# Optimization experiments

Measured on AMD Instinct MI355X. Metric: run time of the kernel, lower is better.

## Reference

```python
import jax, jax.numpy as jnp
import numpy as np

DIM = 1024
NUM_HEADS = 16
HEAD_DIM = DIM // NUM_HEADS
SCALE = HEAD_DIM ** -0.5


def setup_inputs() -> dict:
    key = jax.random.key(0)
    ks = jax.random.split(key, 6)
    B, N = 2, 2048
    s = DIM ** -0.5
    return {
        "x": jax.random.normal(ks[0], (B, N, DIM), dtype=jnp.float32),
        "Wq": jax.random.normal(ks[1], (DIM, DIM), dtype=jnp.float32) * s,
        "Wk": jax.random.normal(ks[2], (DIM, DIM), dtype=jnp.float32) * s,
        "Wv": jax.random.normal(ks[3], (DIM, DIM), dtype=jnp.float32) * s,
        "Wp": jax.random.normal(ks[4], (DIM, DIM), dtype=jnp.float32) * s,
        "bp": jax.random.normal(ks[5], (DIM,), dtype=jnp.float32) * 0.01,
    }


def reference(x, Wq, Wk, Wv, Wp, bp):
    B, N, C = x.shape
    H, D = NUM_HEADS, HEAD_DIM
    # projections (torch Linear: x @ W.T); reshape to (B, H, N, D)
    q = (x @ Wq.T).reshape(B, N, H, D).transpose(0, 2, 1, 3)
    k = (x @ Wk.T).reshape(B, N, H, D).transpose(0, 2, 1, 3)
    v = (x @ Wv.T).reshape(B, N, H, D).transpose(0, 2, 1, 3)
    attn = jnp.einsum("bhnd,bhmd->bhnm", q, k) * SCALE
    attn = jax.nn.softmax(attn, axis=-1)  # dropout p=0 -> identity
    out = jnp.einsum("bhnm,bhmd->bhnd", attn, v)
    out = out.transpose(0, 2, 1, 3).reshape(B, N, C)
    return out @ Wp.T + bp
```

## Files before the change

kernel.cpp:

```cpp
#include <hip/hip_runtime.h>
#include <cstdint>

#define DIMC   1024
#define NHEADS 16
#define HD     64
#define BATCH  2
#define SEQ    2048
#define MROWS  (BATCH*SEQ)
#define QSCALE2 0.18033688f

typedef __bf16 bf16x8 __attribute__((ext_vector_type(8)));
typedef float  f32x4  __attribute__((ext_vector_type(4)));

#define AST 88
#define TST 136

__device__ __forceinline__ unsigned short f2bf(float f) {
    union { float f; unsigned int u; } v; v.f = f;
    unsigned int u = v.u;
    u += 0x7fffu + ((u >> 16) & 1u);
    return (unsigned short)(u >> 16);
}

__device__ __forceinline__ unsigned int pk2bf(float a, float b) {
    union { float f; unsigned int u; } ua, ub;
    ua.f = a; ub.f = b;
    return __builtin_amdgcn_perm(ub.u + 0x8000u, ua.u + 0x8000u, 0x07060302u);
}

__device__ __forceinline__ void gload_lds16(const void* g, void* l) {
    __builtin_amdgcn_global_load_lds(
        (const __attribute__((address_space(1))) unsigned int*)g,
        (__attribute__((address_space(3))) unsigned int*)l, 16, 0, 0);
}

__global__ __launch_bounds__(256) void cast_all(
    const float* __restrict__ x,
    const float* __restrict__ Wq, const float* __restrict__ Wk,
    const float* __restrict__ Wv, const float* __restrict__ Wp,
    unsigned short* __restrict__ xb, unsigned short* __restrict__ Wb)
{
    const size_t M1 = (size_t)DIMC * DIMC;
    int y = blockIdx.y;
    const float* src;
    unsigned short* dst;
    if (y < 4)      { src = x  + (size_t)y * M1; dst = xb + (size_t)y * M1; }
    else if (y == 4){ src = Wq; dst = Wb; }
    else if (y == 5){ src = Wk; dst = Wb + M1; }
    else if (y == 6){ src = Wv; dst = Wb + 2 * M1; }
    else            { src = Wp; dst = Wb + 3 * M1; }
    size_t idx = ((size_t)blockIdx.x * 256 + threadIdx.x) * 4;
    float4 v = *(const float4*)(src + idx);
    ushort4 p; p.x = f2bf(v.x); p.y = f2bf(v.y); p.z = f2bf(v.z); p.w = f2bf(v.w);
    *(ushort4*)(dst + idx) = p;
}

__device__ __forceinline__ void gemm_issue(
    const unsigned short* __restrict__ A, const unsigned short* __restrict__ B,
    unsigned short* As, unsigned short* Bs, int m0, int n0, int kt)
{
    const int t = threadIdx.x;
    const int w = t >> 6, lane = t & 63;
    const int srow = lane >> 3, scol = lane & 7;
#pragma unroll
    for (int i = 0; i < 4; ++i) {
        int r  = i * 32 + w * 8 + srow;
        int cg = scol ^ (r & 7);
        gload_lds16(A + (size_t)(m0 + r) * DIMC + kt + cg * 8, As + r * 64 + scol * 8);
    }
#pragma unroll
    for (int i = 0; i < 2; ++i) {
        int r  = i * 32 + w * 8 + srow;
        int cg = scol ^ (r & 7);
        gload_lds16(B + (size_t)(n0 + r) * DIMC + kt + cg * 8, Bs + r * 64 + scol * 8);
    }
}

__device__ __forceinline__ void gemm_compute(
    const unsigned short* As, const unsigned short* Bs, f32x4 acc[4][2])
{
    const int t = threadIdx.x;
    const int w = t >> 6, lane = t & 63, quad = lane >> 4, lr = lane & 15;
    const int wr = w >> 1, wc = w & 1;
#pragma unroll
    for (int kk = 0; kk < 2; ++kk) {
        bf16x8 af[4], bfr[2];
#pragma unroll
        for (int mt = 0; mt < 4; ++mt) {
            int row = wr * 64 + mt * 16 + lr;
            int cb  = kk * 4 + quad;
            af[mt] = *(const bf16x8*)&As[row * 64 + (cb ^ (row & 7)) * 8];
        }
#pragma unroll
        for (int nt = 0; nt < 2; ++nt) {
            int row = wc * 32 + nt * 16 + lr;
            int cb  = kk * 4 + quad;
            bfr[nt] = *(const bf16x8*)&Bs[row * 64 + (cb ^ (row & 7)) * 8];
        }
#pragma unroll
        for (int mt = 0; mt < 4; ++mt)
#pragma unroll
            for (int nt = 0; nt < 2; ++nt)
                acc[mt][nt] = __builtin_amdgcn_mfma_f32_16x16x32_bf16(af[mt], bfr[nt], acc[mt][nt], 0, 0, 0);
    }
}

__device__ __forceinline__ void gemm_k_loop_db(
    const unsigned short* __restrict__ A, const unsigned short* __restrict__ B,
    unsigned short* smem, int m0, int n0, f32x4 acc[4][2])
{
    unsigned short* As0 = smem;
    unsigned short* Bs0 = smem + 8192;
    unsigned short* As1 = smem + 12288;
    unsigned short* Bs1 = smem + 20480;

    gemm_issue(A, B, As0, Bs0, m0, n0, 0);
    for (int kt = 0; kt < DIMC; kt += 128) {
        __syncthreads();
        gemm_issue(A, B, As1, Bs1, m0, n0, kt + 64);
        gemm_compute(As0, Bs0, acc);
        __syncthreads();
        if (kt + 128 < DIMC) gemm_issue(A, B, As0, Bs0, m0, n0, kt + 128);
        gemm_compute(As1, Bs1, acc);
    }
}

__device__ __forceinline__ void vt_epilogue(
    unsigned short* Ts, f32x4 acc[4][2], int m0, int n0,
    unsigned short* __restrict__ vT)
{
    const int t = threadIdx.x;
    const int w = t >> 6, lane = t & 63, quad = lane >> 4, lr = lane & 15;
    const int wr = w >> 1, wc = w & 1;

    __syncthreads();
#pragma unroll
    for (int mt = 0; mt < 4; ++mt)
#pragma unroll
        for (int nt = 0; nt < 2; ++nt) {
            int lcol  = wc * 32 + nt * 16 + lr;
            int lrow0 = wr * 64 + mt * 16 + quad * 4;
            ushort4 p;
            p.x = f2bf(acc[mt][nt][0]); p.y = f2bf(acc[mt][nt][1]);
            p.z = f2bf(acc[mt][nt][2]); p.w = f2bf(acc[mt][nt][3]);
            *(ushort4*)&Ts[lcol * TST + lrow0] = p;
        }
    __syncthreads();

    int lc = t >> 2, part = t & 3;
    int cg = n0 + lc, hh = cg >> 6, dd = cg & 63;
    int bb = m0 >> 11, nn0 = m0 & (SEQ - 1);
    size_t dst = ((size_t)((bb * NHEADS + hh) * HD + dd)) * SEQ + nn0 + part * 32;
    const unsigned short* srcp = &Ts[lc * TST + part * 32];
#pragma unroll
    for (int i = 0; i < 4; ++i)
        *(uint4*)&vT[dst + i * 8] = *(const uint4*)&srcp[i * 8];
}

__global__ __launch_bounds__(256, 3) void gemm_qkv_fast(
    const unsigned short* __restrict__ xb, const unsigned short* __restrict__ Wb,
    unsigned short* __restrict__ qo, unsigned short* __restrict__ ko,
    unsigned short* __restrict__ vT)
{
    __shared__ unsigned short smem[24576];

    const int t  = threadIdx.x;
    const int lin = blockIdx.y * 16 + blockIdx.x;
    const int T   = (lin & 7) * 64 + (lin >> 3);
    const int n0 = (T & 15) * 64, m0 = (T >> 4) * 128, z = blockIdx.z;
    const unsigned short* B = Wb + (size_t)z * DIMC * DIMC;
    const int w = t >> 6, lane = t & 63, quad = lane >> 4, lr = lane & 15;
    const int wr = w >> 1, wc = w & 1;

    f32x4 acc[4][2];
#pragma unroll
    for (int mt = 0; mt < 4; ++mt)
#pragma unroll
        for (int nt = 0; nt < 2; ++nt)
#pragma unroll
            for (int r = 0; r < 4; ++r) acc[mt][nt][r] = 0.f;

    gemm_k_loop_db(xb, B, smem, m0, n0, acc);

    if (z == 2) {
        vt_epilogue(smem, acc, m0, n0, vT);
    } else {
        unsigned short* Out = (z == 0) ? qo : ko;
        const float sc = (z == 0) ? QSCALE2 : 1.0f;
#pragma unroll
        for (int mt = 0; mt < 4; ++mt)
#pragma unroll
            for (int nt = 0; nt < 2; ++nt)
#pragma unroll
                for (int r = 0; r < 4; ++r) {
                    int row = m0 + wr * 64 + mt * 16 + quad * 4 + r;
                    int col = n0 + wc * 32 + nt * 16 + lr;
                    Out[(size_t)row * DIMC + col] = f2bf(acc[mt][nt][r] * sc);
                }
    }
}

__global__ __launch_bounds__(256, 3) void gemm_out_fast(
    const unsigned short* __restrict__ O, const unsigned short* __restrict__ Wpb,
    const float* __restrict__ bias, float* __restrict__ out)
{
    __shared__ unsigned short smem[24576];

    const int t  = threadIdx.x;
    const int lin = blockIdx.y * 16 + blockIdx.x;
    const int T   = (lin & 7) * 64 + (lin >> 3);
    const int n0 = (T & 15) * 64, m0 = (T >> 4) * 128;
    const int w = t >> 6, lane = t & 63, quad = lane >> 4, lr = lane & 15;
    const int wr = w >> 1, wc = w & 1;

    f32x4 acc[4][2];
#pragma unroll
    for (int mt = 0; mt < 4; ++mt)
#pragma unroll
        for (int nt = 0; nt < 2; ++nt)
#pragma unroll
            for (int r = 0; r < 4; ++r) acc[mt][nt][r] = 0.f;

    gemm_k_loop_db(O, Wpb, smem, m0, n0, acc);

#pragma unroll
    for (int mt = 0; mt < 4; ++mt)
#pragma unroll
        for (int nt = 0; nt < 2; ++nt)
#pragma unroll
            for (int r = 0; r < 4; ++r) {
                int row = m0 + wr * 64 + mt * 16 + quad * 4 + r;
                int col = n0 + wc * 32 + nt * 16 + lr;
                out[(size_t)row * DIMC + col] = acc[mt][nt][r] + bias[col];
            }
}

__global__ __launch_bounds__(256, 2) void attn_kernel(
    const unsigned short* __restrict__ qg, const unsigned short* __restrict__ kg,
    const unsigned short* __restrict__ vT, unsigned short* __restrict__ og)
{
    __shared__ unsigned short Ka[64 * 64];
    __shared__ unsigned short Kb[64 * 64];
    __shared__ unsigned short Va[64 * 64];
    __shared__ unsigned short Vb[64 * 64];
    __shared__ unsigned short PsA[128 * 64];
    __shared__ unsigned short PsB[128 * 64];

    const int t  = threadIdx.x;
    const int w = t >> 6, l = t & 63, quad = l >> 4, lr = l & 15;
    const int srow = t >> 3, scol = t & 7;
    const int pkey = (lr & 7) << 1;

    const int bid  = blockIdx.x;
    const int slot = bid >> 3;
    const int bh   = (bid & 7) * 4 + (slot >> 4);
    const int qt   = slot & 15;
    const int b    = bh >> 4, h = bh & 15;

    const unsigned short* khead = kg + ((size_t)(b * SEQ)) * DIMC + h * HD;
    const unsigned short* vhead = vT + (size_t)((b * NHEADS + h) * HD) * SEQ;

    bf16x8 qf[2][2];
#pragma unroll
    for (int mt = 0; mt < 2; ++mt) {
        const size_t qoff = ((size_t)(b * SEQ + qt * 128 + w * 32 + mt * 16 + lr)) * DIMC + h * HD;
        qf[mt][0] = *(const bf16x8*)(qg + qoff + 0  + quad * 8);
        qf[mt][1] = *(const bf16x8*)(qg + qoff + 32 + quad * 8);
    }

    bf16x8 ones;
#pragma unroll
    for (int j = 0; j < 8; ++j) ones[j] = (__bf16)1.0f;
    const f32x4 fzero = { 0.f, 0.f, 0.f, 0.f };

    f32x4 o_acc[2][4], lacc[2];
#pragma unroll
    for (int mt = 0; mt < 2; ++mt) {
        lacc[mt] = fzero;
#pragma unroll
        for (int ct = 0; ct < 4; ++ct) o_acc[mt][ct] = fzero;
    }

    auto issue = [&](int kt, unsigned short* Kd, unsigned short* Vd) {
#pragma unroll
        for (int i = 0; i < 2; ++i) {
            int r  = i * 32 + srow;
            int cg = scol ^ (r & 7);
            gload_lds16(khead + (size_t)(kt * 64 + r) * DIMC + cg * 8, Kd + r * 64 + scol * 8);
            gload_lds16(vhead + (size_t)r * SEQ + kt * 64 + cg * 8,   Vd + r * 64 + scol * 8);
        }
    };

    auto s_phase = [&](const unsigned short* Kc, f32x4 (&s)[2][4]) {
        __builtin_amdgcn_s_setprio(1);
#pragma unroll
        for (int nt = 0; nt < 4; ++nt) {
            int row = nt * 16 + lr;
            bf16x8 kf = *(const bf16x8*)&Kc[row * 64 + ((quad ^ (row & 7)) * 8)];
#pragma unroll
            for (int mt = 0; mt < 2; ++mt)
                s[mt][nt] = __builtin_amdgcn_mfma_f32_16x16x32_bf16(kf, qf[mt][0], fzero, 0, 0, 0);
        }
#pragma unroll
        for (int nt = 0; nt < 4; ++nt) {
            int row = nt * 16 + lr;
            bf16x8 kf = *(const bf16x8*)&Kc[row * 64 + (((4 + quad) ^ (row & 7)) * 8)];
#pragma unroll
            for (int mt = 0; mt < 2; ++mt)
                s[mt][nt] = __builtin_amdgcn_mfma_f32_16x16x32_bf16(kf, qf[mt][1], s[mt][nt], 0, 0, 0);
        }
        __builtin_amdgcn_s_setprio(0);
    };

    auto exp_store = [&](const f32x4 (&s)[2][4], unsigned short* PsW) {
#pragma unroll
        for (int mt = 0; mt < 2; ++mt)
#pragma unroll
            for (int nt = 0; nt < 4; ++nt) {
                uint2 pp;
                pp.x = pk2bf(__builtin_amdgcn_exp2f(s[mt][nt][0]),
                             __builtin_amdgcn_exp2f(s[mt][nt][1]));
                pp.y = pk2bf(__builtin_amdgcn_exp2f(s[mt][nt][2]),
                             __builtin_amdgcn_exp2f(s[mt][nt][3]));
                *(uint2*)&PsW[(w * 32 + mt * 16 + lr) * 64 + (((nt * 4 + quad) ^ pkey) * 4)] = pp;
            }
    };

    auto vload = [&](const unsigned short* Vc, bf16x8 (&vr)[8]) {
#pragma unroll
        for (int kk = 0; kk < 2; ++kk)
#pragma unroll
            for (int ct = 0; ct < 4; ++ct) {
                int row = ct * 16 + lr;
                vr[kk * 4 + ct] = *(const bf16x8*)&Vc[row * 64 + (((kk * 4 + quad) ^ (row & 7)) * 8)];
            }
    };

    auto pv = [&](const unsigned short* PsR, const bf16x8 (&vr)[8]) {
        __builtin_amdgcn_s_setprio(1);
#pragma unroll
        for (int kk = 0; kk < 2; ++kk)
#pragma unroll
            for (int mt = 0; mt < 2; ++mt) {
                bf16x8 pf = *(const bf16x8*)&PsR[(w * 32 + mt * 16 + lr) * 64 + (((kk * 8 + quad * 2) ^ pkey) * 4)];
                lacc[mt] = __builtin_amdgcn_mfma_f32_16x16x32_bf16(pf, ones, lacc[mt], 0, 0, 0);
#pragma unroll
                for (int ct = 0; ct < 4; ++ct)
                    o_acc[mt][ct] = __builtin_amdgcn_mfma_f32_16x16x32_bf16(pf, vr[kk * 4 + ct], o_acc[mt][ct], 0, 0, 0);
            }
        __builtin_amdgcn_s_setprio(0);
    };

    bf16x8 vrA[8], vrB[8];

    issue(0, Ka, Va);
    for (int kt = 0; kt < SEQ / 64; kt += 2) {
        __syncthreads();
        issue(kt + 1, Kb, Vb);
        {
            f32x4 s[2][4];
            s_phase(Ka, s);
            if (kt) pv(PsB, vrB);
            exp_store(s, PsA);
            vload(Va, vrA);
        }
        __syncthreads();
        if (kt + 2 < SEQ / 64) issue(kt + 2, Ka, Va);
        {
            f32x4 s[2][4];
            s_phase(Kb, s);
            pv(PsA, vrA);
            exp_store(s, PsB);
            vload(Vb, vrB);
        }
    }
    pv(PsB, vrB);

#pragma unroll
    for (int mt = 0; mt < 2; ++mt) {
        float inv[4];
#pragma unroll
        for (int r = 0; r < 4; ++r) inv[r] = 1.0f / lacc[mt][r];
#pragma unroll
        for (int ct = 0; ct < 4; ++ct)
#pragma unroll
            for (int r = 0; r < 4; ++r) {
                int qrow = qt * 128 + w * 32 + mt * 16 + quad * 4 + r;
                og[((size_t)(b * SEQ + qrow)) * DIMC + h * HD + ct * 16 + lr] =
                    f2bf(o_acc[mt][ct][r] * inv[r]);
            }
    }
}

__global__ __launch_bounds__(256) void gemm_qkv_f32(
    const float* __restrict__ x,
    const float* __restrict__ Wq, const float* __restrict__ Wk, const float* __restrict__ Wv,
    unsigned short* __restrict__ qo, unsigned short* __restrict__ ko, unsigned short* __restrict__ vT)
{
    __shared__ unsigned short smem[2 * 128 * AST];
    unsigned short* As = smem;
    unsigned short* Bs = smem + 128 * AST;

    const int t  = threadIdx.x;
    const int n0 = blockIdx.x * 128, m0 = blockIdx.y * 128, z = blockIdx.z;
    const float* W = (z == 0) ? Wq : (z == 1) ? Wk : Wv;
    const int w = t >> 6, l = t & 63, quad = l >> 4, lr = l & 15;
    const int wr = w >> 1, wc = w & 1;

    f32x4 acc[4][4];
#pragma unroll
    for (int mt = 0; mt < 4; ++mt)
#pragma unroll
        for (int nt = 0; nt < 4; ++nt)
#pragma unroll
            for (int r = 0; r < 4; ++r) acc[mt][nt][r] = 0.f;

    for (int kt = 0; kt < DIMC; kt += 64) {
        __syncthreads();
#pragma unroll
        for (int i = 0; i < 8; ++i) {
            int flat = t + i * 256;
            int row = flat >> 4, seg = flat & 15;
            float4 a = *(const float4*)(x + (size_t)(m0 + row) * DIMC + kt + seg * 4);
            ushort4 pa; pa.x = f2bf(a.x); pa.y = f2bf(a.y); pa.z = f2bf(a.z); pa.w = f2bf(a.w);
            *(ushort4*)&As[row * AST + seg * 4] = pa;
            float4 b = *(const float4*)(W + (size_t)(n0 + row) * DIMC + kt + seg * 4);
            ushort4 pb; pb.x = f2bf(b.x); pb.y = f2bf(b.y); pb.z = f2bf(b.z); pb.w = f2bf(b.w);
            *(ushort4*)&Bs[row * AST + seg * 4] = pb;
        }
        __syncthreads();
#pragma unroll
        for (int kk = 0; kk < 2; ++kk) {
            bf16x8 af[4], bfr[4];
#pragma unroll
            for (int mt = 0; mt < 4; ++mt)
                af[mt] = *(const bf16x8*)&As[(wr * 64 + mt * 16 + lr) * AST + kk * 32 + quad * 8];
#pragma unroll
            for (int nt = 0; nt < 4; ++nt)
                bfr[nt] = *(const bf16x8*)&Bs[(wc * 64 + nt * 16 + lr) * AST + kk * 32 + quad * 8];
#pragma unroll
            for (int mt = 0; mt < 4; ++mt)
#pragma unroll
                for (int nt = 0; nt < 4; ++nt)
                    acc[mt][nt] = __builtin_amdgcn_mfma_f32_16x16x32_bf16(af[mt], bfr[nt], acc[mt][nt], 0, 0, 0);
        }
    }

    if (z == 2) {
        __syncthreads();
#pragma unroll
        for (int mt = 0; mt < 4; ++mt)
#pragma unroll
            for (int nt = 0; nt < 4; ++nt) {
                int lcol  = wc * 64 + nt * 16 + lr;
                int lrow0 = wr * 64 + mt * 16 + quad * 4;
                ushort4 p;
                p.x = f2bf(acc[mt][nt][0]); p.y = f2bf(acc[mt][nt][1]);
                p.z = f2bf(acc[mt][nt][2]); p.w = f2bf(acc[mt][nt][3]);
                *(ushort4*)&smem[lcol * TST + lrow0] = p;
            }
        __syncthreads();
        int lc = t >> 1, half = t & 1;
        int cg = n0 + lc, hh = cg >> 6, dd = cg & 63;
        int bb = m0 >> 11, nn0 = m0 & (SEQ - 1);
        size_t dst = ((size_t)((bb * NHEADS + hh) * HD + dd)) * SEQ + nn0 + half * 64;
        const unsigned short* srcp = &smem[lc * TST + half * 64];
#pragma unroll
        for (int i = 0; i < 8; ++i)
            *(uint4*)&vT[dst + i * 8] = *(const uint4*)&srcp[i * 8];
    } else {
        unsigned short* Out = (z == 0) ? qo : ko;
        const float sc = (z == 0) ? QSCALE2 : 1.0f;
#pragma unroll
        for (int mt = 0; mt < 4; ++mt)
#pragma unroll
            for (int nt = 0; nt < 4; ++nt)
#pragma unroll
                for (int r = 0; r < 4; ++r) {
                    int row = m0 + wr * 64 + mt * 16 + quad * 4 + r;
                    int col = n0 + wc * 64 + nt * 16 + lr;
                    Out[(size_t)row * DIMC + col] = f2bf(acc[mt][nt][r] * sc);
                }
    }
}

__global__ __launch_bounds__(256) void gemm_out_f32(
    const unsigned short* __restrict__ A, const float* __restrict__ Wp,
    const float* __restrict__ bias, float* __restrict__ out)
{
    __shared__ unsigned short As[128 * AST];
    __shared__ unsigned short Bs[128 * AST];

    const int t  = threadIdx.x;
    const int n0 = blockIdx.x * 128, m0 = blockIdx.y * 128;
    const int w = t >> 6, l = t & 63, quad = l >> 4, lr = l & 15;
    const int wr = w >> 1, wc = w & 1;

    f32x4 acc[4][4];
#pragma unroll
    for (int mt = 0; mt < 4; ++mt)
#pragma unroll
        for (int nt = 0; nt < 4; ++nt)
#pragma unroll
            for (int r = 0; r < 4; ++r) acc[mt][nt][r] = 0.f;

    for (int kt = 0; kt < DIMC; kt += 64) {
        __syncthreads();
#pragma unroll
        for (int i = 0; i < 8; ++i) {
            int flat = t + i * 256;
            int row = flat >> 4, seg = flat & 15;
            ushort4 a = *(const ushort4*)(A + (size_t)(m0 + row) * DIMC + kt + seg * 4);
            *(ushort4*)&As[row * AST + seg * 4] = a;
            float4 b = *(const float4*)(Wp + (size_t)(n0 + row) * DIMC + kt + seg * 4);
            ushort4 pb; pb.x = f2bf(b.x); pb.y = f2bf(b.y); pb.z = f2bf(b.z); pb.w = f2bf(b.w);
            *(ushort4*)&Bs[row * AST + seg * 4] = pb;
        }
        __syncthreads();
#pragma unroll
        for (int kk = 0; kk < 2; ++kk) {
            bf16x8 af[4], bfr[4];
#pragma unroll
            for (int mt = 0; mt < 4; ++mt)
                af[mt] = *(const bf16x8*)&As[(wr * 64 + mt * 16 + lr) * AST + kk * 32 + quad * 8];
#pragma unroll
            for (int nt = 0; nt < 4; ++nt)
                bfr[nt] = *(const bf16x8*)&Bs[(wc * 64 + nt * 16 + lr) * AST + kk * 32 + quad * 8];
#pragma unroll
            for (int mt = 0; mt < 4; ++mt)
#pragma unroll
                for (int nt = 0; nt < 4; ++nt)
                    acc[mt][nt] = __builtin_amdgcn_mfma_f32_16x16x32_bf16(af[mt], bfr[nt], acc[mt][nt], 0, 0, 0);
        }
    }

#pragma unroll
    for (int mt = 0; mt < 4; ++mt)
#pragma unroll
        for (int nt = 0; nt < 4; ++nt)
#pragma unroll
            for (int r = 0; r < 4; ++r) {
                int row = m0 + wr * 64 + mt * 16 + quad * 4 + r;
                int col = n0 + wc * 64 + nt * 16 + lr;
                out[(size_t)row * DIMC + col] = acc[mt][nt][r] + bias[col];
            }
}

extern "C" void kernel_launch(void* const* d_in, const int* in_sizes, int n_in,
                              void* d_out, int out_size, void* d_ws, size_t ws_size,
                              hipStream_t stream)
{
    const float* x  = (const float*)d_in[0];
    const float* Wq = (const float*)d_in[1];
    const float* Wk = (const float*)d_in[2];
    const float* Wv = (const float*)d_in[3];
    const float* Wp = (const float*)d_in[4];
    const float* bp = (const float*)d_in[5];
    float* out = (float*)d_out;

    const size_t SZ  = (size_t)MROWS * DIMC;
    const size_t WSZ = (size_t)DIMC * DIMC;
    const size_t need = (4 * SZ + 4 * WSZ) * sizeof(unsigned short);

    if (ws_size >= need) {
        unsigned short* q  = (unsigned short*)d_ws;
        unsigned short* k  = q + SZ;
        unsigned short* vt = k + SZ;
        unsigned short* o  = vt + SZ;
        unsigned short* Wb = o + SZ;
        unsigned short* xb = (unsigned short*)d_out;

        cast_all<<<dim3(1024, 8), 256, 0, stream>>>(x, Wq, Wk, Wv, Wp, xb, Wb);
        gemm_qkv_fast<<<dim3(16, 32, 3), 256, 0, stream>>>(xb, Wb, q, k, vt);
        attn_kernel<<<dim3(512), 256, 0, stream>>>(q, k, vt, o);
        gemm_out_fast<<<dim3(16, 32), 256, 0, stream>>>(o, Wb + 3 * WSZ, bp, out);
    } else {
        unsigned short* q  = (unsigned short*)d_ws;
        unsigned short* k  = q + SZ;
        unsigned short* vt = k + SZ;
        unsigned short* o  = vt + SZ;

        gemm_qkv_f32<<<dim3(DIMC / 128, MROWS / 128, 3), 256, 0, stream>>>(x, Wq, Wk, Wv, q, k, vt);
        attn_kernel<<<dim3(512), 256, 0, stream>>>(q, k, vt, o);
        gemm_out_f32<<<dim3(DIMC / 128, MROWS / 128), 256, 0, stream>>>(o, Wp, bp, out);
    }
}
```

Baseline: 172.5 us.

## Enlarge QKV GEMM tile to 128x128 with 32-wide K steps

The QKV projection GEMM now uses 128x128 output tiles per block instead of 128x64, with each wave computing a 64x64 sub-tile (4x4 MFMAs) and a K-step of 32 using a new paired-row swizzled LDS layout. The aim is more arithmetic per loaded byte and fewer blocks, halving B-tile reloads across the grid. The V-transpose epilogue is adapted to the wider tile, and the output projection GEMM keeps the old 128x64 path as separate copies. Costs include more accumulator registers, which may hurt occupancy, and twice as many barriers per K because the K-step is halved.

```diff
diff --git a/kernel.cpp b/kernel.cpp
--- a/kernel.cpp
+++ b/kernel.cpp
@@ -55,78 +55,70 @@
     *(ushort4*)(dst + idx) = p;
 }
 
-__device__ __forceinline__ void gemm_issue(
+__device__ __forceinline__ void gemm_issue32(
     const unsigned short* __restrict__ A, const unsigned short* __restrict__ B,
     unsigned short* As, unsigned short* Bs, int m0, int n0, int kt)
 {
     const int t = threadIdx.x;
-    const int w = t >> 6, lane = t & 63;
-    const int srow = lane >> 3, scol = lane & 7;
-#pragma unroll
-    for (int i = 0; i < 4; ++i) {
-        int r  = i * 32 + w * 8 + srow;
-        int cg = scol ^ (r & 7);
-        gload_lds16(A + (size_t)(m0 + r) * DIMC + kt + cg * 8, As + r * 64 + scol * 8);
-    }
+    const int rr = t >> 2, cg = t & 3;
 #pragma unroll
     for (int i = 0; i < 2; ++i) {
-        int r  = i * 32 + w * 8 + srow;
-        int cg = scol ^ (r & 7);
-        gload_lds16(B + (size_t)(n0 + r) * DIMC + kt + cg * 8, Bs + r * 64 + scol * 8);
-    }
-}
-
-__device__ __forceinline__ void gemm_compute(
-    const unsigned short* As, const unsigned short* Bs, f32x4 acc[4][2])
+        int r  = i * 64 + rr;
+        int sc = cg ^ ((r >> 1) & 3);
+        int dst = (r >> 1) * 64 + (r & 1) * 32 + cg * 8;
+        gload_lds16(A + (size_t)(m0 + r) * DIMC + kt + sc * 8, As + dst);
+        gload_lds16(B + (size_t)(n0 + r) * DIMC + kt + sc * 8, Bs + dst);
+    }
+}
+
+__device__ __forceinline__ void gemm_compute32(
+    const unsigned short* As, const unsigned short* Bs, f32x4 acc[4][4])
 {
     const int t = threadIdx.x;
     const int w = t >> 6, lane = t & 63, quad = lane >> 4, lr = lane & 15;
     const int wr = w >> 1, wc = w & 1;
-#pragma unroll
-    for (int kk = 0; kk < 2; ++kk) {
-        bf16x8 af[4], bfr[2];
-#pragma unroll
-        for (int mt = 0; mt < 4; ++mt) {
-            int row = wr * 64 + mt * 16 + lr;
-            int cb  = kk * 4 + quad;
-            af[mt] = *(const bf16x8*)&As[row * 64 + (cb ^ (row & 7)) * 8];
-        }
-#pragma unroll
-        for (int nt = 0; nt < 2; ++nt) {
-            int row = wc * 32 + nt * 16 + lr;
-            int cb  = kk * 4 + quad;
-            bfr[nt] = *(const bf16x8*)&Bs[row * 64 + (cb ^ (row & 7)) * 8];
-        }
-#pragma unroll
-        for (int mt = 0; mt < 4; ++mt)
-#pragma unroll
-            for (int nt = 0; nt < 2; ++nt)
-                acc[mt][nt] = __builtin_amdgcn_mfma_f32_16x16x32_bf16(af[mt], bfr[nt], acc[mt][nt], 0, 0, 0);
-    }
-}
-
-__device__ __forceinline__ void gemm_k_loop_db(
+    bf16x8 af[4], bfr[4];
+#pragma unroll
+    for (int mt = 0; mt < 4; ++mt) {
+        int row = wr * 64 + mt * 16 + lr;
+        af[mt] = *(const bf16x8*)&As[(row >> 1) * 64 + (row & 1) * 32
+                                     + ((quad ^ ((row >> 1) & 3)) * 8)];
+    }
+#pragma unroll
+    for (int nt = 0; nt < 4; ++nt) {
+        int row = wc * 64 + nt * 16 + lr;
+        bfr[nt] = *(const bf16x8*)&Bs[(row >> 1) * 64 + (row & 1) * 32
+                                      + ((quad ^ ((row >> 1) & 3)) * 8)];
+    }
+#pragma unroll
+    for (int mt = 0; mt < 4; ++mt)
+#pragma unroll
+        for (int nt = 0; nt < 4; ++nt)
+            acc[mt][nt] = __builtin_amdgcn_mfma_f32_16x16x32_bf16(af[mt], bfr[nt], acc[mt][nt], 0, 0, 0);
+}
+
+__device__ __forceinline__ void gemm_k_loop_db32(
     const unsigned short* __restrict__ A, const unsigned short* __restrict__ B,
-    unsigned short* smem, int m0, int n0, f32x4 acc[4][2])
+    unsigned short* smem, int m0, int n0, f32x4 acc[4][4])
 {
     unsigned short* As0 = smem;
-    unsigned short* Bs0 = smem + 8192;
-    unsigned short* As1 = smem + 12288;
-    unsigned short* Bs1 = smem + 20480;
-
-    gemm_issue(A, B, As0, Bs0, m0, n0, 0);
-    for (int kt = 0; kt < DIMC; kt += 128) {
-        __syncthreads();
-        gemm_issue(A, B, As1, Bs1, m0, n0, kt + 64);
-        gemm_compute(As0, Bs0, acc);
-        __syncthreads();
-        if (kt + 128 < DIMC) gemm_issue(A, B, As0, Bs0, m0, n0, kt + 128);
-        gemm_compute(As1, Bs1, acc);
+    unsigned short* Bs0 = smem + 4096;
+    unsigned short* As1 = smem + 8192;
+    unsigned short* Bs1 = smem + 12288;
+
+    gemm_issue32(A, B, As0, Bs0, m0, n0, 0);
+    for (int kt = 0; kt < DIMC; kt += 64) {
+        __syncthreads();
+        gemm_issue32(A, B, As1, Bs1, m0, n0, kt + 32);
+        gemm_compute32(As0, Bs0, acc);
+        __syncthreads();
+        if (kt + 64 < DIMC) gemm_issue32(A, B, As0, Bs0, m0, n0, kt + 64);
+        gemm_compute32(As1, Bs1, acc);
     }
 }
 
 __device__ __forceinline__ void vt_epilogue(
-    unsigned short* Ts, f32x4 acc[4][2], int m0, int n0,
+    unsigned short* Ts, f32x4 acc[4][4], int m0, int n0,
     unsigned short* __restrict__ vT)
 {
     const int t = threadIdx.x;
@@ -137,8 +129,8 @@
 #pragma unroll
     for (int mt = 0; mt < 4; ++mt)
 #pragma unroll
-        for (int nt = 0; nt < 2; ++nt) {
-            int lcol  = wc * 32 + nt * 16 + lr;
+        for (int nt = 0; nt < 4; ++nt) {
+            int lcol  = wc * 64 + nt * 16 + lr;
             int lrow0 = wr * 64 + mt * 16 + quad * 4;
             ushort4 p;
             p.x = f2bf(acc[mt][nt][0]); p.y = f2bf(acc[mt][nt][1]);
@@ -147,13 +139,13 @@
         }
     __syncthreads();
 
-    int lc = t >> 2, part = t & 3;
+    int lc = t >> 1, half = t & 1;
     int cg = n0 + lc, hh = cg >> 6, dd = cg & 63;
     int bb = m0 >> 11, nn0 = m0 & (SEQ - 1);
-    size_t dst = ((size_t)((bb * NHEADS + hh) * HD + dd)) * SEQ + nn0 + part * 32;
-    const unsigned short* srcp = &Ts[lc * TST + part * 32];
-#pragma unroll
-    for (int i = 0; i < 4; ++i)
+    size_t dst = ((size_t)((bb * NHEADS + hh) * HD + dd)) * SEQ + nn0 + half * 64;
+    const unsigned short* srcp = &Ts[lc * TST + half * 64];
+#pragma unroll
+    for (int i = 0; i < 8; ++i)
         *(uint4*)&vT[dst + i * 8] = *(const uint4*)&srcp[i * 8];
 }
 
@@ -162,25 +154,25 @@
     unsigned short* __restrict__ qo, unsigned short* __restrict__ ko,
     unsigned short* __restrict__ vT)
 {
-    __shared__ unsigned short smem[24576];
+    __shared__ unsigned short smem[17408];
 
     const int t  = threadIdx.x;
-    const int lin = blockIdx.y * 16 + blockIdx.x;
-    const int T   = (lin & 7) * 64 + (lin >> 3);
-    const int n0 = (T & 15) * 64, m0 = (T >> 4) * 128, z = blockIdx.z;
+    const int lin = blockIdx.y * 8 + blockIdx.x;
+    const int T   = (lin & 7) * 32 + (lin >> 3);
+    const int n0 = (T & 7) * 128, m0 = (T >> 3) * 128, z = blockIdx.z;
     const unsigned short* B = Wb + (size_t)z * DIMC * DIMC;
     const int w = t >> 6, lane = t & 63, quad = lane >> 4, lr = lane & 15;
     const int wr = w >> 1, wc = w & 1;
 
-    f32x4 acc[4][2];
-#pragma unroll
-    for (int mt = 0; mt < 4; ++mt)
-#pragma unroll
-        for (int nt = 0; nt < 2; ++nt)
+    f32x4 acc[4][4];
+#pragma unroll
+    for (int mt = 0; mt < 4; ++mt)
+#pragma unroll
+        for (int nt = 0; nt < 4; ++nt)
 #pragma unroll
             for (int r = 0; r < 4; ++r) acc[mt][nt][r] = 0.f;
 
-    gemm_k_loop_db(xb, B, smem, m0, n0, acc);
+    gemm_k_loop_db32(xb, B, smem, m0, n0, acc);
 
     if (z == 2) {
         vt_epilogue(smem, acc, m0, n0, vT);
@@ -190,13 +182,63 @@
 #pragma unroll
         for (int mt = 0; mt < 4; ++mt)
 #pragma unroll
-            for (int nt = 0; nt < 2; ++nt)
+            for (int nt = 0; nt < 4; ++nt)
 #pragma unroll
                 for (int r = 0; r < 4; ++r) {
                     int row = m0 + wr * 64 + mt * 16 + quad * 4 + r;
-                    int col = n0 + wc * 32 + nt * 16 + lr;
+                    int col = n0 + wc * 64 + nt * 16 + lr;
                     Out[(size_t)row * DIMC + col] = f2bf(acc[mt][nt][r] * sc);
                 }
+    }
+}
+
+__device__ __forceinline__ void gemm_issue_out(
+    const unsigned short* __restrict__ A, const unsigned short* __restrict__ B,
+    unsigned short* As, unsigned short* Bs, int m0, int n0, int kt)
+{
+    const int t = threadIdx.x;
+    const int w = t >> 6, lane = t & 63;
+    const int srow = lane >> 3, scol = lane & 7;
+#pragma unroll
+    for (int i = 0; i < 4; ++i) {
+        int r  = i * 32 + w * 8 + srow;
+        int cg = scol ^ (r & 7);
+        gload_lds16(A + (size_t)(m0 + r) * DIMC + kt + cg * 8, As + r * 64 + scol * 8);
+    }
+#pragma unroll
+    for (int i = 0; i < 2; ++i) {
+        int r  = i * 32 + w * 8 + srow;
+        int cg = scol ^ (r & 7);
+        gload_lds16(B + (size_t)(n0 + r) * DIMC + kt + cg * 8, Bs + r * 64 + scol * 8);
+    }
+}
+
+__device__ __forceinline__ void gemm_compute_out(
+    const unsigned short* As, const unsigned short* Bs, f32x4 acc[4][2])
+{
+    const int t = threadIdx.x;
+    const int w = t >> 6, lane = t & 63, quad = lane >> 4, lr = lane & 15;
+    const int wr = w >> 1, wc = w & 1;
+#pragma unroll
+    for (int kk = 0; kk < 2; ++kk) {
+        bf16x8 af[4], bfr[2];
+#pragma unroll
+        for (int mt = 0; mt < 4; ++mt) {
+            int row = wr * 64 + mt * 16 + lr;
+            int cb  = kk * 4 + quad;
+            af[mt] = *(const bf16x8*)&As[row * 64 + (cb ^ (row & 7)) * 8];
+        }
+#pragma unroll
+        for (int nt = 0; nt < 2; ++nt) {
+            int row = wc * 32 + nt * 16 + lr;
+            int cb  = kk * 4 + quad;
+            bfr[nt] = *(const bf16x8*)&Bs[row * 64 + (cb ^ (row & 7)) * 8];
+        }
+#pragma unroll
+        for (int mt = 0; mt < 4; ++mt)
+#pragma unroll
+            for (int nt = 0; nt < 2; ++nt)
+                acc[mt][nt] = __builtin_amdgcn_mfma_f32_16x16x32_bf16(af[mt], bfr[nt], acc[mt][nt], 0, 0, 0);
     }
 }
 
@@ -221,7 +263,20 @@
 #pragma unroll
             for (int r = 0; r < 4; ++r) acc[mt][nt][r] = 0.f;
 
-    gemm_k_loop_db(O, Wpb, smem, m0, n0, acc);
+    unsigned short* As0 = smem;
+    unsigned short* Bs0 = smem + 8192;
+    unsigned short* As1 = smem + 12288;
+    unsigned short* Bs1 = smem + 20480;
+
+    gemm_issue_out(O, Wpb, As0, Bs0, m0, n0, 0);
+    for (int kt = 0; kt < DIMC; kt += 128) {
+        __syncthreads();
+        gemm_issue_out(O, Wpb, As1, Bs1, m0, n0, kt + 64);
+        gemm_compute_out(As0, Bs0, acc);
+        __syncthreads();
+        if (kt + 128 < DIMC) gemm_issue_out(O, Wpb, As0, Bs0, m0, n0, kt + 128);
+        gemm_compute_out(As1, Bs1, acc);
+    }
 
 #pragma unroll
     for (int mt = 0; mt < 4; ++mt)
@@ -571,7 +626,7 @@
         unsigned short* xb = (unsigned short*)d_out;
 
         cast_all<<<dim3(1024, 8), 256, 0, stream>>>(x, Wq, Wk, Wv, Wp, xb, Wb);
-        gemm_qkv_fast<<<dim3(16, 32, 3), 256, 0, stream>>>(xb, Wb, q, k, vt);
+        gemm_qkv_fast<<<dim3(8, 32, 3), 256, 0, stream>>>(xb, Wb, q, k, vt);
         attn_kernel<<<dim3(512), 256, 0, stream>>>(q, k, vt, o);
         gemm_out_fast<<<dim3(16, 32), 256, 0, stream>>>(o, Wb + 3 * WSZ, bp, out);
     } else {
```

Result: no change. 172.0 us (-0.3%).
